# Optimization experiments

Hardware: AMD Instinct MI355X
Metric: run time of the kernel (lower is better)

Reference implementation:

```python
import jax, jax.numpy as jnp
import numpy as np

EMB = 512
N_ROWS = 10000
N_PAIRS = 65536


def setup_inputs() -> dict:
    key = jax.random.key(0)
    ks = jax.random.split(key, 10)
    s1 = 1.0 / np.sqrt(2 * EMB)
    s2 = 1.0 / np.sqrt(128)
    s3 = 1.0 / np.sqrt(64)
    return {
        "pos_pairs": jax.random.randint(ks[0], (N_PAIRS, 3), 0, N_ROWS, dtype=jnp.int32),
        "neg_pairs": jax.random.randint(ks[1], (N_PAIRS, 3), 0, N_ROWS, dtype=jnp.int32),
        "drug_embedding": jax.random.normal(ks[2], (N_ROWS, EMB), dtype=jnp.float32),
        "target_embedding": jax.random.normal(ks[3], (N_ROWS, EMB), dtype=jnp.float32),
        "W1": jax.random.normal(ks[4], (2 * EMB, 128), dtype=jnp.float32) * s1,
        "b1": jnp.zeros((128,), dtype=jnp.float32),
        "W2": jax.random.normal(ks[5], (128, 64), dtype=jnp.float32) * s2,
        "b2": jnp.zeros((64,), dtype=jnp.float32),
        "W3": jax.random.normal(ks[6], (64, 1), dtype=jnp.float32) * s3,
        "b3": jnp.zeros((1,), dtype=jnp.float32),
    }


def _mlp(x, W1, b1, W2, b2, W3, b3):
    h = jax.nn.relu(x @ W1 + b1)
    h = jax.nn.relu(h @ W2 + b2)
    return (h @ W3 + b3)[..., 0]  # [N]


def _pair_loss(pairs, drug_emb, tgt_emb, W1, b1, W2, b2, W3, b3):
    d = drug_emb[pairs[:, 0]]            # [N, EMB]
    t1 = tgt_emb[pairs[:, 1]]            # [N, EMB]
    t2 = tgt_emb[pairs[:, 2]]            # [N, EMB]
    a1 = _mlp(jnp.concatenate([d, t1], axis=-1), W1, b1, W2, b2, W3, b3)
    a2 = _mlp(jnp.concatenate([d, t2], axis=-1), W1, b1, W2, b2, W3, b3)
    # per-pair MSE of scalar affinities = (a1 - a2)^2; mean over pairs
    return jnp.mean((a1 - a2) ** 2)


def reference(pos_pairs, neg_pairs, drug_embedding, target_embedding,
              W1, b1, W2, b2, W3, b3):
    pos = _pair_loss(pos_pairs, drug_embedding, target_embedding, W1, b1, W2, b2, W3, b3)
    neg = _pair_loss(neg_pairs, drug_embedding, target_embedding, W1, b1, W2, b2, W3, b3)
    return pos - neg
```

## Files before the change

### kernel.cpp

```cpp
#include <hip/hip_runtime.h>

#define EMB 512
#define NROWS 10000
#define NPAIRS 65536

typedef __bf16 bf16x8 __attribute__((ext_vector_type(8)));
typedef float  f32x4  __attribute__((ext_vector_type(4)));
typedef unsigned int u32x4 __attribute__((ext_vector_type(4)));

__device__ __forceinline__ void split2(float x0, float x1, unsigned* hw, unsigned* lw) {
    unsigned u0 = __float_as_uint(x0), u1 = __float_as_uint(x1);
    unsigned r0 = u0 + 0x7FFFu + ((u0 >> 16) & 1u);
    unsigned r1 = u1 + 0x7FFFu + ((u1 >> 16) & 1u);
    float h0 = __uint_as_float(r0 & 0xFFFF0000u);
    float h1 = __uint_as_float(r1 & 0xFFFF0000u);
    float l0 = x0 - h0, l1 = x1 - h1;
    unsigned v0 = __float_as_uint(l0), v1 = __float_as_uint(l1);
    unsigned s0 = v0 + 0x7FFFu + ((v0 >> 16) & 1u);
    unsigned s1 = v1 + 0x7FFFu + ((v1 >> 16) & 1u);
    *hw = (r0 >> 16) | (r1 & 0xFFFF0000u);
    *lw = (s0 >> 16) | (s1 & 0xFFFF0000u);
}

__global__ __launch_bounds__(256)
void k0_fragment(const float* __restrict__ W1, const float* __restrict__ W2,
                 unsigned short* __restrict__ W1Fhi, unsigned short* __restrict__ W1Flo,
                 unsigned short* __restrict__ W2Fhi, unsigned short* __restrict__ W2Flo)
{
    int e = blockIdx.x * 256 + threadIdx.x;
    float x;
    unsigned short *hp, *lp;
    if (e < 131072) {
        int i  = e & 7;
        int l  = (e >> 3) & 63;
        int nt = (e >> 9) & 7;
        int kt = (e >> 12) & 15;
        int t  = e >> 16;
        int k = kt * 32 + 8 * (l >> 4) + i;
        int n = nt * 16 + (l & 15);
        x = W1[(t * 512 + k) * 128 + n];
        hp = W1Fhi + e; lp = W1Flo + e;
    } else {
        int e2 = e - 131072;
        int i  = e2 & 7;
        int l  = (e2 >> 3) & 63;
        int nt = (e2 >> 9) & 3;
        int kt = e2 >> 11;
        int k = kt * 32 + 8 * (l >> 4) + i;
        int n = nt * 16 + (l & 15);
        x = W2[k * 64 + n];
        hp = W2Fhi + e2; lp = W2Flo + e2;
    }
    unsigned u = __float_as_uint(x);
    unsigned r = u + 0x7FFFu + ((u >> 16) & 1u);
    float hf = __uint_as_float(r & 0xFFFF0000u);
    float lf = x - hf;
    unsigned v = __float_as_uint(lf);
    unsigned s = v + 0x7FFFu + ((v >> 16) & 1u);
    *hp = (unsigned short)(r >> 16);
    *lp = (unsigned short)(s >> 16);
}

#define K1_TILES 625

__global__ __launch_bounds__(256, 4)
void k1_mfma(const float* __restrict__ drug, const float* __restrict__ tgt,
             const unsigned* __restrict__ W1Fhi, const unsigned* __restrict__ W1Flo,
             const float* __restrict__ b1,
             float* __restrict__ D, float* __restrict__ T)
{
    __shared__ unsigned short Ahi[16][512];
    __shared__ unsigned short Alo[16][512];

    int bid = blockIdx.x, tid = threadIdx.x;
    bool isT = bid >= K1_TILES;
    int rt = isT ? bid - K1_TILES : bid;
    const float* emb = isT ? tgt : drug;
    float* out = isT ? T : D;
    int row0 = rt * 16;

    int wave = tid >> 6, lane = tid & 63;
    int g = lane >> 4, lm = lane & 15;
    int ntb = wave * 2;

    float4 va[4][2];
    #pragma unroll
    for (int i = 0; i < 4; i++) {
        const float* src = emb + (size_t)(row0 + wave * 4 + i) * EMB + lane * 8;
        va[i][0] = *(const float4*)src;
        va[i][1] = *(const float4*)(src + 4);
    }
    #pragma unroll
    for (int i = 0; i < 4; i++) {
        int row = wave * 4 + i;
        unsigned h0, h1, h2, h3, l0, l1, l2, l3;
        split2(va[i][0].x, va[i][0].y, &h0, &l0);
        split2(va[i][0].z, va[i][0].w, &h1, &l1);
        split2(va[i][1].x, va[i][1].y, &h2, &l2);
        split2(va[i][1].z, va[i][1].w, &h3, &l3);
        u32x4 hq, lq;
        hq[0]=h0; hq[1]=h1; hq[2]=h2; hq[3]=h3;
        lq[0]=l0; lq[1]=l1; lq[2]=l2; lq[3]=l3;
        int c = lane ^ (row & 7);
        *(u32x4*)((char*)&Ahi[0][0] + row * 1024 + c * 16) = hq;
        *(u32x4*)((char*)&Alo[0][0] + row * 1024 + c * 16) = lq;
    }
    __syncthreads();

    const u32x4* BH = (const u32x4*)W1Fhi + (isT ? 8192 : 0);
    const u32x4* BL = (const u32x4*)W1Flo + (isT ? 8192 : 0);

    f32x4 acc[2];
    #pragma unroll
    for (int j = 0; j < 2; j++) { acc[j][0]=0.f; acc[j][1]=0.f; acc[j][2]=0.f; acc[j][3]=0.f; }

    #pragma unroll
    for (int kt = 0; kt < 16; kt++) {
        u32x4 bh0 = BH[(kt * 8 + ntb) * 64 + lane];
        u32x4 bh1 = BH[(kt * 8 + ntb + 1) * 64 + lane];
        u32x4 bl0 = BL[(kt * 8 + ntb) * 64 + lane];
        u32x4 bl1 = BL[(kt * 8 + ntb + 1) * 64 + lane];
        int c = (kt * 4 + g) ^ (lm & 7);
        u32x4 ahq = *(const u32x4*)((const char*)&Ahi[0][0] + lm * 1024 + c * 16);
        u32x4 alq = *(const u32x4*)((const char*)&Alo[0][0] + lm * 1024 + c * 16);
        bf16x8 Ah = __builtin_bit_cast(bf16x8, ahq);
        bf16x8 Al = __builtin_bit_cast(bf16x8, alq);
        bf16x8 Bh0 = __builtin_bit_cast(bf16x8, bh0);
        bf16x8 Bh1 = __builtin_bit_cast(bf16x8, bh1);
        bf16x8 Bl0 = __builtin_bit_cast(bf16x8, bl0);
        bf16x8 Bl1 = __builtin_bit_cast(bf16x8, bl1);
        acc[0] = __builtin_amdgcn_mfma_f32_16x16x32_bf16(Ah, Bh0, acc[0], 0, 0, 0);
        acc[1] = __builtin_amdgcn_mfma_f32_16x16x32_bf16(Ah, Bh1, acc[1], 0, 0, 0);
        acc[0] = __builtin_amdgcn_mfma_f32_16x16x32_bf16(Ah, Bl0, acc[0], 0, 0, 0);
        acc[1] = __builtin_amdgcn_mfma_f32_16x16x32_bf16(Ah, Bl1, acc[1], 0, 0, 0);
        acc[0] = __builtin_amdgcn_mfma_f32_16x16x32_bf16(Al, Bh0, acc[0], 0, 0, 0);
        acc[1] = __builtin_amdgcn_mfma_f32_16x16x32_bf16(Al, Bh1, acc[1], 0, 0, 0);
    }

    #pragma unroll
    for (int j = 0; j < 2; j++) {
        int col = (ntb + j) * 16 + lm;
        float bias = isT ? 0.f : b1[col];
        #pragma unroll
        for (int reg = 0; reg < 4; reg++) {
            int row = row0 + 4 * g + reg;
            out[row * 128 + col] = acc[j][reg] + bias;
        }
    }
}

__global__ __launch_bounds__(256)
void k2_pairs(const float* __restrict__ D, const float* __restrict__ T,
              const int* __restrict__ pos, const int* __restrict__ neg,
              const unsigned* __restrict__ W2Fhi, const unsigned* __restrict__ W2Flo,
              const float* __restrict__ b2, const float* __restrict__ W3,
              double* __restrict__ partials)
{
    __shared__ u32x4 Ash[4][768];

    int tid = threadIdx.x;
    int wave = tid >> 6, lane = tid & 63;
    int g = lane >> 4, lm = lane & 15;
    int rr = lane >> 3, cc = lane & 7;
    int gw = blockIdx.x * 4 + wave;
    const int* pairs = (gw < 2048) ? pos : neg;
    int p0 = (gw & 2047) * 32;

    const float* bp[12];
    #pragma unroll
    for (int it = 0; it < 12; it++) {
        int pr = it * 8 + rr;
        int idxv;
        const float* src;
        if (pr < 32) { idxv = pairs[(p0 + pr) * 3]; src = D; }
        else { int q = pr - 32; idxv = pairs[(p0 + (q >> 1)) * 3 + 1 + (q & 1)]; src = T; }
        bp[it] = src + (size_t)idxv * 128 + ((cc ^ (pr & 7)) << 2);
    }

    u32x4* A4w = &Ash[wave][0];
    const u32x4* BH4 = (const u32x4*)W2Fhi;
    const u32x4* BL4 = (const u32x4*)W2Flo;

    f32x4 acc[4][4];
    #pragma unroll
    for (int mt = 0; mt < 4; mt++)
        #pragma unroll
        for (int nt = 0; nt < 4; nt++) { acc[mt][nt][0]=0.f; acc[mt][nt][1]=0.f; acc[mt][nt][2]=0.f; acc[mt][nt][3]=0.f; }

    #pragma unroll 1
    for (int kt = 0; kt < 4; kt++) {
        u32x4 bh[4], bl[4];
        #pragma unroll
        for (int nt = 0; nt < 4; nt++) {
            bh[nt] = BH4[(kt * 4 + nt) * 64 + lane];
            bl[nt] = BL4[(kt * 4 + nt) * 64 + lane];
        }
        #pragma unroll
        for (int it = 0; it < 12; it++) {
            __builtin_amdgcn_global_load_lds(
                (const __attribute__((address_space(1))) void*)(bp[it] + kt * 32),
                (__attribute__((address_space(3))) void*)((char*)A4w + it * 1024),
                16, 0, 0);
        }
        asm volatile("s_waitcnt vmcnt(0)" ::: "memory");
        #pragma unroll
        for (int mt = 0; mt < 4; mt++) {
            int r = mt * 16 + lm;
            int p = r >> 1;
            int ds = p & 7, ts = r & 7;
            const f32x4* drow = (const f32x4*)(A4w + p * 8);
            const f32x4* trow = (const f32x4*)(A4w + (32 + r) * 8);
            f32x4 d0 = drow[(2 * g) ^ ds];
            f32x4 d1 = drow[(2 * g + 1) ^ ds];
            f32x4 t0 = trow[(2 * g) ^ ts];
            f32x4 t1 = trow[(2 * g + 1) ^ ts];
            float h0 = fmaxf(d0[0] + t0[0], 0.f), h1v = fmaxf(d0[1] + t0[1], 0.f);
            float h2 = fmaxf(d0[2] + t0[2], 0.f), h3 = fmaxf(d0[3] + t0[3], 0.f);
            float h4 = fmaxf(d1[0] + t1[0], 0.f), h5 = fmaxf(d1[1] + t1[1], 0.f);
            float h6 = fmaxf(d1[2] + t1[2], 0.f), h7 = fmaxf(d1[3] + t1[3], 0.f);
            unsigned hq0, hq1, hq2, hq3, lq0, lq1, lq2, lq3;
            split2(h0, h1v, &hq0, &lq0);
            split2(h2, h3,  &hq1, &lq1);
            split2(h4, h5,  &hq2, &lq2);
            split2(h6, h7,  &hq3, &lq3);
            u32x4 ah, al;
            ah[0]=hq0; ah[1]=hq1; ah[2]=hq2; ah[3]=hq3;
            al[0]=lq0; al[1]=lq1; al[2]=lq2; al[3]=lq3;
            bf16x8 Ah = __builtin_bit_cast(bf16x8, ah);
            bf16x8 Al = __builtin_bit_cast(bf16x8, al);
            #pragma unroll
            for (int nt = 0; nt < 4; nt++) {
                bf16x8 Bh = __builtin_bit_cast(bf16x8, bh[nt]);
                bf16x8 Bl = __builtin_bit_cast(bf16x8, bl[nt]);
                acc[mt][nt] = __builtin_amdgcn_mfma_f32_16x16x32_bf16(Ah, Bh, acc[mt][nt], 0, 0, 0);
                acc[mt][nt] = __builtin_amdgcn_mfma_f32_16x16x32_bf16(Ah, Bl, acc[mt][nt], 0, 0, 0);
                acc[mt][nt] = __builtin_amdgcn_mfma_f32_16x16x32_bf16(Al, Bh, acc[mt][nt], 0, 0, 0);
            }
        }
        asm volatile("s_waitcnt lgkmcnt(0)" ::: "memory");
    }

    float b2v[4], w3v[4];
    #pragma unroll
    for (int nt = 0; nt < 4; nt++) { b2v[nt] = b2[nt * 16 + lm]; w3v[nt] = W3[nt * 16 + lm]; }

    float pr[4][4];
    #pragma unroll
    for (int mt = 0; mt < 4; mt++)
        #pragma unroll
        for (int reg = 0; reg < 4; reg++) {
            float s = 0.f;
            #pragma unroll
            for (int nt = 0; nt < 4; nt++) {
                float h2 = fmaxf(acc[mt][nt][reg] + b2v[nt], 0.f);
                s = fmaf(h2, w3v[nt], s);
            }
            pr[mt][reg] = s;
        }
    #pragma unroll
    for (int m = 1; m <= 8; m <<= 1)
        #pragma unroll
        for (int mt = 0; mt < 4; mt++)
            #pragma unroll
            for (int reg = 0; reg < 4; reg++)
                pr[mt][reg] += __shfl_xor(pr[mt][reg], m, 64);

    double dsq = 0.0;
    #pragma unroll
    for (int mt = 0; mt < 4; mt++) {
        float d0 = pr[mt][0] - pr[mt][1];
        float d1 = pr[mt][2] - pr[mt][3];
        dsq += (double)d0 * (double)d0 + (double)d1 * (double)d1;
    }
    dsq += __shfl_xor(dsq, 16, 64);
    dsq += __shfl_xor(dsq, 32, 64);

    __syncthreads();
    if (lane == 0) ((double*)&Ash[wave][0])[0] = dsq;
    __syncthreads();
    if (tid == 0) {
        double sum = 0.0;
        #pragma unroll
        for (int w = 0; w < 4; w++) sum += ((double*)&Ash[w][0])[0];
        partials[blockIdx.x] = sum;
    }
}

__global__ void k3_final(const double* __restrict__ partials, float* __restrict__ out)
{
    int lane = threadIdx.x;
    double sp = 0.0, sn = 0.0;
    #pragma unroll
    for (int i = 0; i < 8; i++) {
        sp += partials[lane + 64 * i];
        sn += partials[512 + lane + 64 * i];
    }
    #pragma unroll
    for (int m = 1; m <= 32; m <<= 1) {
        sp += __shfl_xor(sp, m, 64);
        sn += __shfl_xor(sn, m, 64);
    }
    if (lane == 0) out[0] = (float)((sp - sn) / (double)NPAIRS);
}

extern "C" void kernel_launch(void* const* d_in, const int* in_sizes, int n_in,
                              void* d_out, int out_size, void* d_ws, size_t ws_size,
                              hipStream_t stream) {
    const int*   pos  = (const int*)d_in[0];
    const int*   neg  = (const int*)d_in[1];
    const float* drug = (const float*)d_in[2];
    const float* tgt  = (const float*)d_in[3];
    const float* W1   = (const float*)d_in[4];
    const float* b1   = (const float*)d_in[5];
    const float* W2   = (const float*)d_in[6];
    const float* b2   = (const float*)d_in[7];
    const float* W3   = (const float*)d_in[8];

    float* Dp = (float*)d_ws;
    float* Tp = Dp + NROWS * 128;
    char* base = (char*)(Tp + NROWS * 128);
    unsigned short* W2Fhi = (unsigned short*)base;
    unsigned short* W2Flo = W2Fhi + 8192;
    unsigned short* W1Fhi = W2Flo + 8192;
    unsigned short* W1Flo = W1Fhi + 131072;
    double* partials = (double*)(W1Flo + 131072);
    float* out = (float*)d_out;

    k0_fragment<<<544, 256, 0, stream>>>(W1, W2, W1Fhi, W1Flo, W2Fhi, W2Flo);
    k1_mfma<<<2 * K1_TILES, 256, 0, stream>>>(drug, tgt, (const unsigned*)W1Fhi,
                                              (const unsigned*)W1Flo, b1, Dp, Tp);
    k2_pairs<<<1024, 256, 0, stream>>>(Dp, Tp, pos, neg, (const unsigned*)W2Fhi,
                                       (const unsigned*)W2Flo, b2, W3, partials);
    k3_final<<<1, 64, 0, stream>>>(partials, out);
}
```

Measured before the change: 60.10 us.

## Keep W1 fragments in registers across multiple row chunks with double-buffered LDS

Result: faster. 58.03 us (-3.4%).

```diff
diff --git a/kernel.cpp b/kernel.cpp
--- a/kernel.cpp
+++ b/kernel.cpp
@@ -61,91 +61,104 @@
     *lp = (unsigned short)(s >> 16);
 }
 
-#define K1_TILES 625
-
-__global__ __launch_bounds__(256, 4)
+#define K1_RPB 79
+#define K1_NCH 5
+
+__global__ __launch_bounds__(256, 2)
 void k1_mfma(const float* __restrict__ drug, const float* __restrict__ tgt,
              const unsigned* __restrict__ W1Fhi, const unsigned* __restrict__ W1Flo,
              const float* __restrict__ b1,
              float* __restrict__ D, float* __restrict__ T)
 {
-    __shared__ unsigned short Ahi[16][512];
-    __shared__ unsigned short Alo[16][512];
+    __shared__ unsigned short Ah[2][16][512];
+    __shared__ unsigned short Al[2][16][512];
 
     int bid = blockIdx.x, tid = threadIdx.x;
-    bool isT = bid >= K1_TILES;
-    int rt = isT ? bid - K1_TILES : bid;
-    const float* emb = isT ? tgt : drug;
-    float* out = isT ? T : D;
-    int row0 = rt * 16;
+    int t  = bid & 1;
+    int ch = (bid >> 1) & 1;
+    int rg = bid >> 2;
+    const float* emb = t ? tgt : drug;
+    float* out = t ? T : D;
+    int row_base = rg * K1_RPB;
 
     int wave = tid >> 6, lane = tid & 63;
     int g = lane >> 4, lm = lane & 15;
-    int ntb = wave * 2;
+    int nt = ch * 4 + wave;
+
+    const u32x4* BH = (const u32x4*)W1Fhi + (t ? 8192 : 0);
+    const u32x4* BL = (const u32x4*)W1Flo + (t ? 8192 : 0);
+
+    u32x4 bhv[16], blv[16];
+    #pragma unroll
+    for (int kt = 0; kt < 16; kt++) {
+        bhv[kt] = BH[(kt * 8 + nt) * 64 + lane];
+        blv[kt] = BL[(kt * 8 + nt) * 64 + lane];
+    }
+    float bias = t ? 0.f : b1[nt * 16 + lm];
 
     float4 va[4][2];
     #pragma unroll
     for (int i = 0; i < 4; i++) {
-        const float* src = emb + (size_t)(row0 + wave * 4 + i) * EMB + lane * 8;
+        int gr = row_base + 0 * 16 + wave * 4 + i;
+        if (gr > NROWS - 1) gr = NROWS - 1;
+        const float* src = emb + (size_t)gr * EMB + lane * 8;
         va[i][0] = *(const float4*)src;
         va[i][1] = *(const float4*)(src + 4);
     }
-    #pragma unroll
-    for (int i = 0; i < 4; i++) {
-        int row = wave * 4 + i;
-        unsigned h0, h1, h2, h3, l0, l1, l2, l3;
-        split2(va[i][0].x, va[i][0].y, &h0, &l0);
-        split2(va[i][0].z, va[i][0].w, &h1, &l1);
-        split2(va[i][1].x, va[i][1].y, &h2, &l2);
-        split2(va[i][1].z, va[i][1].w, &h3, &l3);
-        u32x4 hq, lq;
-        hq[0]=h0; hq[1]=h1; hq[2]=h2; hq[3]=h3;
-        lq[0]=l0; lq[1]=l1; lq[2]=l2; lq[3]=l3;
-        int c = lane ^ (row & 7);
-        *(u32x4*)((char*)&Ahi[0][0] + row * 1024 + c * 16) = hq;
-        *(u32x4*)((char*)&Alo[0][0] + row * 1024 + c * 16) = lq;
-    }
-    __syncthreads();
-
-    const u32x4* BH = (const u32x4*)W1Fhi + (isT ? 8192 : 0);
-    const u32x4* BL = (const u32x4*)W1Flo + (isT ? 8192 : 0);
-
-    f32x4 acc[2];
-    #pragma unroll
-    for (int j = 0; j < 2; j++) { acc[j][0]=0.f; acc[j][1]=0.f; acc[j][2]=0.f; acc[j][3]=0.f; }
-
-    #pragma unroll
-    for (int kt = 0; kt < 16; kt++) {
-        u32x4 bh0 = BH[(kt * 8 + ntb) * 64 + lane];
-        u32x4 bh1 = BH[(kt * 8 + ntb + 1) * 64 + lane];
-        u32x4 bl0 = BL[(kt * 8 + ntb) * 64 + lane];
-        u32x4 bl1 = BL[(kt * 8 + ntb + 1) * 64 + lane];
-        int c = (kt * 4 + g) ^ (lm & 7);
-        u32x4 ahq = *(const u32x4*)((const char*)&Ahi[0][0] + lm * 1024 + c * 16);
-        u32x4 alq = *(const u32x4*)((const char*)&Alo[0][0] + lm * 1024 + c * 16);
-        bf16x8 Ah = __builtin_bit_cast(bf16x8, ahq);
-        bf16x8 Al = __builtin_bit_cast(bf16x8, alq);
-        bf16x8 Bh0 = __builtin_bit_cast(bf16x8, bh0);
-        bf16x8 Bh1 = __builtin_bit_cast(bf16x8, bh1);
-        bf16x8 Bl0 = __builtin_bit_cast(bf16x8, bl0);
-        bf16x8 Bl1 = __builtin_bit_cast(bf16x8, bl1);
-        acc[0] = __builtin_amdgcn_mfma_f32_16x16x32_bf16(Ah, Bh0, acc[0], 0, 0, 0);
-        acc[1] = __builtin_amdgcn_mfma_f32_16x16x32_bf16(Ah, Bh1, acc[1], 0, 0, 0);
-        acc[0] = __builtin_amdgcn_mfma_f32_16x16x32_bf16(Ah, Bl0, acc[0], 0, 0, 0);
-        acc[1] = __builtin_amdgcn_mfma_f32_16x16x32_bf16(Ah, Bl1, acc[1], 0, 0, 0);
-        acc[0] = __builtin_amdgcn_mfma_f32_16x16x32_bf16(Al, Bh0, acc[0], 0, 0, 0);
-        acc[1] = __builtin_amdgcn_mfma_f32_16x16x32_bf16(Al, Bh1, acc[1], 0, 0, 0);
-    }
-
-    #pragma unroll
-    for (int j = 0; j < 2; j++) {
-        int col = (ntb + j) * 16 + lm;
-        float bias = isT ? 0.f : b1[col];
+
+    #pragma unroll
+    for (int c = 0; c < K1_NCH; c++) {
+        float4 vb[4][2];
+        if (c + 1 < K1_NCH) {
+            #pragma unroll
+            for (int i = 0; i < 4; i++) {
+                int gr = row_base + (c + 1) * 16 + wave * 4 + i;
+                if (gr > NROWS - 1) gr = NROWS - 1;
+                const float* src = emb + (size_t)gr * EMB + lane * 8;
+                vb[i][0] = *(const float4*)src;
+                vb[i][1] = *(const float4*)(src + 4);
+            }
+        }
+        #pragma unroll
+        for (int i = 0; i < 4; i++) {
+            int lr = wave * 4 + i;
+            unsigned h0, h1, h2, h3, l0, l1, l2, l3;
+            split2(va[i][0].x, va[i][0].y, &h0, &l0);
+            split2(va[i][0].z, va[i][0].w, &h1, &l1);
+            split2(va[i][1].x, va[i][1].y, &h2, &l2);
+            split2(va[i][1].z, va[i][1].w, &h3, &l3);
+            u32x4 hq, lq;
+            hq[0]=h0; hq[1]=h1; hq[2]=h2; hq[3]=h3;
+            lq[0]=l0; lq[1]=l1; lq[2]=l2; lq[3]=l3;
+            int cc = lane ^ (lr & 7);
+            *(u32x4*)((char*)&Ah[c & 1][0][0] + lr * 1024 + cc * 16) = hq;
+            *(u32x4*)((char*)&Al[c & 1][0][0] + lr * 1024 + cc * 16) = lq;
+        }
+        __syncthreads();
+        f32x4 acc;
+        acc[0]=0.f; acc[1]=0.f; acc[2]=0.f; acc[3]=0.f;
+        #pragma unroll
+        for (int kt = 0; kt < 16; kt++) {
+            int cc = (kt * 4 + g) ^ (lm & 7);
+            u32x4 ahq = *(const u32x4*)((const char*)&Ah[c & 1][0][0] + lm * 1024 + cc * 16);
+            u32x4 alq = *(const u32x4*)((const char*)&Al[c & 1][0][0] + lm * 1024 + cc * 16);
+            bf16x8 Af = __builtin_bit_cast(bf16x8, ahq);
+            bf16x8 Alf = __builtin_bit_cast(bf16x8, alq);
+            bf16x8 Bh = __builtin_bit_cast(bf16x8, bhv[kt]);
+            bf16x8 Bl = __builtin_bit_cast(bf16x8, blv[kt]);
+            acc = __builtin_amdgcn_mfma_f32_16x16x32_bf16(Af, Bh, acc, 0, 0, 0);
+            acc = __builtin_amdgcn_mfma_f32_16x16x32_bf16(Af, Bl, acc, 0, 0, 0);
+            acc = __builtin_amdgcn_mfma_f32_16x16x32_bf16(Alf, Bh, acc, 0, 0, 0);
+        }
         #pragma unroll
         for (int reg = 0; reg < 4; reg++) {
-            int row = row0 + 4 * g + reg;
-            out[row * 128 + col] = acc[j][reg] + bias;
-        }
+            int lr = c * 16 + 4 * g + reg;
+            int row = row_base + lr;
+            if (lr < K1_RPB && row < NROWS)
+                out[row * 128 + nt * 16 + lm] = acc[reg] + bias;
+        }
+        #pragma unroll
+        for (int i = 0; i < 4; i++) { va[i][0] = vb[i][0]; va[i][1] = vb[i][1]; }
     }
 }
 
@@ -226,15 +239,15 @@
             u32x4 ah, al;
             ah[0]=hq0; ah[1]=hq1; ah[2]=hq2; ah[3]=hq3;
             al[0]=lq0; al[1]=lq1; al[2]=lq2; al[3]=lq3;
-            bf16x8 Ah = __builtin_bit_cast(bf16x8, ah);
-            bf16x8 Al = __builtin_bit_cast(bf16x8, al);
+            bf16x8 Ahf = __builtin_bit_cast(bf16x8, ah);
+            bf16x8 Alf = __builtin_bit_cast(bf16x8, al);
             #pragma unroll
             for (int nt = 0; nt < 4; nt++) {
                 bf16x8 Bh = __builtin_bit_cast(bf16x8, bh[nt]);
                 bf16x8 Bl = __builtin_bit_cast(bf16x8, bl[nt]);
-                acc[mt][nt] = __builtin_amdgcn_mfma_f32_16x16x32_bf16(Ah, Bh, acc[mt][nt], 0, 0, 0);
-                acc[mt][nt] = __builtin_amdgcn_mfma_f32_16x16x32_bf16(Ah, Bl, acc[mt][nt], 0, 0, 0);
-                acc[mt][nt] = __builtin_amdgcn_mfma_f32_16x16x32_bf16(Al, Bh, acc[mt][nt], 0, 0, 0);
+                acc[mt][nt] = __builtin_amdgcn_mfma_f32_16x16x32_bf16(Ahf, Bh, acc[mt][nt], 0, 0, 0);
+                acc[mt][nt] = __builtin_amdgcn_mfma_f32_16x16x32_bf16(Ahf, Bl, acc[mt][nt], 0, 0, 0);
+                acc[mt][nt] = __builtin_amdgcn_mfma_f32_16x16x32_bf16(Alf, Bh, acc[mt][nt], 0, 0, 0);
             }
         }
         asm volatile("s_waitcnt lgkmcnt(0)" ::: "memory");
@@ -327,8 +340,8 @@
     float* out = (float*)d_out;
 
     k0_fragment<<<544, 256, 0, stream>>>(W1, W2, W1Fhi, W1Flo, W2Fhi, W2Flo);
-    k1_mfma<<<2 * K1_TILES, 256, 0, stream>>>(drug, tgt, (const unsigned*)W1Fhi,
-                                              (const unsigned*)W1Flo, b1, Dp, Tp);
+    k1_mfma<<<512, 256, 0, stream>>>(drug, tgt, (const unsigned*)W1Fhi,
+                                     (const unsigned*)W1Flo, b1, Dp, Tp);
     k2_pairs<<<1024, 256, 0, stream>>>(Dp, Tp, pos, neg, (const unsigned*)W2Fhi,
                                        (const unsigned*)W2Flo, b2, W3, partials);
     k3_final<<<1, 64, 0, stream>>>(partials, out);
```

## Stream k1 A tiles via global_load_lds per K step with in-loop bf16 split

Applied to the files above, without the earlier changes.

After: 60.60 us. About the same (+0.8%).

```diff
diff --git a/kernel.cpp b/kernel.cpp
--- a/kernel.cpp
+++ b/kernel.cpp
@@ -63,14 +63,13 @@
 
 #define K1_TILES 625
 
-__global__ __launch_bounds__(256, 4)
-void k1_mfma(const float* __restrict__ drug, const float* __restrict__ tgt,
-             const unsigned* __restrict__ W1Fhi, const unsigned* __restrict__ W1Flo,
-             const float* __restrict__ b1,
-             float* __restrict__ D, float* __restrict__ T)
+__global__ __launch_bounds__(256)
+void k1_dma(const float* __restrict__ drug, const float* __restrict__ tgt,
+            const unsigned* __restrict__ W1Fhi, const unsigned* __restrict__ W1Flo,
+            const float* __restrict__ b1,
+            float* __restrict__ D, float* __restrict__ T)
 {
-    __shared__ unsigned short Ahi[16][512];
-    __shared__ unsigned short Alo[16][512];
+    __shared__ u32x4 Abuf[4][128];
 
     int bid = blockIdx.x, tid = threadIdx.x;
     bool isT = bid >= K1_TILES;
@@ -81,50 +80,53 @@
 
     int wave = tid >> 6, lane = tid & 63;
     int g = lane >> 4, lm = lane & 15;
+    int rr = lane >> 3, cc = lane & 7;
     int ntb = wave * 2;
-
-    float4 va[4][2];
-    #pragma unroll
-    for (int i = 0; i < 4; i++) {
-        const float* src = emb + (size_t)(row0 + wave * 4 + i) * EMB + lane * 8;
-        va[i][0] = *(const float4*)src;
-        va[i][1] = *(const float4*)(src + 4);
-    }
-    #pragma unroll
-    for (int i = 0; i < 4; i++) {
-        int row = wave * 4 + i;
-        unsigned h0, h1, h2, h3, l0, l1, l2, l3;
-        split2(va[i][0].x, va[i][0].y, &h0, &l0);
-        split2(va[i][0].z, va[i][0].w, &h1, &l1);
-        split2(va[i][1].x, va[i][1].y, &h2, &l2);
-        split2(va[i][1].z, va[i][1].w, &h3, &l3);
-        u32x4 hq, lq;
-        hq[0]=h0; hq[1]=h1; hq[2]=h2; hq[3]=h3;
-        lq[0]=l0; lq[1]=l1; lq[2]=l2; lq[3]=l3;
-        int c = lane ^ (row & 7);
-        *(u32x4*)((char*)&Ahi[0][0] + row * 1024 + c * 16) = hq;
-        *(u32x4*)((char*)&Alo[0][0] + row * 1024 + c * 16) = lq;
-    }
-    __syncthreads();
+    int rk = lm & 7;
 
     const u32x4* BH = (const u32x4*)W1Fhi + (isT ? 8192 : 0);
     const u32x4* BL = (const u32x4*)W1Flo + (isT ? 8192 : 0);
 
+    const float* sp[2];
+    #pragma unroll
+    for (int it = 0; it < 2; it++) {
+        int pr = it * 8 + rr;
+        sp[it] = emb + (size_t)(row0 + pr) * EMB + ((cc ^ (pr & 7)) << 2);
+    }
+
+    u32x4* A4w = &Abuf[wave][0];
+
     f32x4 acc[2];
     #pragma unroll
     for (int j = 0; j < 2; j++) { acc[j][0]=0.f; acc[j][1]=0.f; acc[j][2]=0.f; acc[j][3]=0.f; }
 
-    #pragma unroll
+    #pragma unroll 1
     for (int kt = 0; kt < 16; kt++) {
         u32x4 bh0 = BH[(kt * 8 + ntb) * 64 + lane];
         u32x4 bh1 = BH[(kt * 8 + ntb + 1) * 64 + lane];
         u32x4 bl0 = BL[(kt * 8 + ntb) * 64 + lane];
         u32x4 bl1 = BL[(kt * 8 + ntb + 1) * 64 + lane];
-        int c = (kt * 4 + g) ^ (lm & 7);
-        u32x4 ahq = *(const u32x4*)((const char*)&Ahi[0][0] + lm * 1024 + c * 16);
-        u32x4 alq = *(const u32x4*)((const char*)&Alo[0][0] + lm * 1024 + c * 16);
-        bf16x8 Ah = __builtin_bit_cast(bf16x8, ahq);
-        bf16x8 Al = __builtin_bit_cast(bf16x8, alq);
+        #pragma unroll
+        for (int it = 0; it < 2; it++) {
+            __builtin_amdgcn_global_load_lds(
+                (const __attribute__((address_space(1))) void*)(sp[it] + kt * 32),
+                (__attribute__((address_space(3))) void*)((char*)A4w + it * 1024),
+                16, 0, 0);
+        }
+        asm volatile("s_waitcnt vmcnt(0)" ::: "memory");
+        const f32x4* Af = (const f32x4*)A4w;
+        f32x4 a0 = Af[lm * 8 + ((2 * g)     ^ rk)];
+        f32x4 a1 = Af[lm * 8 + ((2 * g + 1) ^ rk)];
+        unsigned h0, h1, h2, h3, l0, l1, l2, l3;
+        split2(a0[0], a0[1], &h0, &l0);
+        split2(a0[2], a0[3], &h1, &l1);
+        split2(a1[0], a1[1], &h2, &l2);
+        split2(a1[2], a1[3], &h3, &l3);
+        u32x4 ah, al;
+        ah[0]=h0; ah[1]=h1; ah[2]=h2; ah[3]=h3;
+        al[0]=l0; al[1]=l1; al[2]=l2; al[3]=l3;
+        bf16x8 Ah = __builtin_bit_cast(bf16x8, ah);
+        bf16x8 Al = __builtin_bit_cast(bf16x8, al);
         bf16x8 Bh0 = __builtin_bit_cast(bf16x8, bh0);
         bf16x8 Bh1 = __builtin_bit_cast(bf16x8, bh1);
         bf16x8 Bl0 = __builtin_bit_cast(bf16x8, bl0);
@@ -135,6 +137,7 @@
         acc[1] = __builtin_amdgcn_mfma_f32_16x16x32_bf16(Ah, Bl1, acc[1], 0, 0, 0);
         acc[0] = __builtin_amdgcn_mfma_f32_16x16x32_bf16(Al, Bh0, acc[0], 0, 0, 0);
         acc[1] = __builtin_amdgcn_mfma_f32_16x16x32_bf16(Al, Bh1, acc[1], 0, 0, 0);
+        asm volatile("s_waitcnt lgkmcnt(0)" ::: "memory");
     }
 
     #pragma unroll
@@ -226,15 +229,15 @@
             u32x4 ah, al;
             ah[0]=hq0; ah[1]=hq1; ah[2]=hq2; ah[3]=hq3;
             al[0]=lq0; al[1]=lq1; al[2]=lq2; al[3]=lq3;
-            bf16x8 Ah = __builtin_bit_cast(bf16x8, ah);
-            bf16x8 Al = __builtin_bit_cast(bf16x8, al);
+            bf16x8 Ahf = __builtin_bit_cast(bf16x8, ah);
+            bf16x8 Alf = __builtin_bit_cast(bf16x8, al);
             #pragma unroll
             for (int nt = 0; nt < 4; nt++) {
                 bf16x8 Bh = __builtin_bit_cast(bf16x8, bh[nt]);
                 bf16x8 Bl = __builtin_bit_cast(bf16x8, bl[nt]);
-                acc[mt][nt] = __builtin_amdgcn_mfma_f32_16x16x32_bf16(Ah, Bh, acc[mt][nt], 0, 0, 0);
-                acc[mt][nt] = __builtin_amdgcn_mfma_f32_16x16x32_bf16(Ah, Bl, acc[mt][nt], 0, 0, 0);
-                acc[mt][nt] = __builtin_amdgcn_mfma_f32_16x16x32_bf16(Al, Bh, acc[mt][nt], 0, 0, 0);
+                acc[mt][nt] = __builtin_amdgcn_mfma_f32_16x16x32_bf16(Ahf, Bh, acc[mt][nt], 0, 0, 0);
+                acc[mt][nt] = __builtin_amdgcn_mfma_f32_16x16x32_bf16(Ahf, Bl, acc[mt][nt], 0, 0, 0);
+                acc[mt][nt] = __builtin_amdgcn_mfma_f32_16x16x32_bf16(Alf, Bh, acc[mt][nt], 0, 0, 0);
             }
         }
         asm volatile("s_waitcnt lgkmcnt(0)" ::: "memory");
@@ -327,8 +330,8 @@
     float* out = (float*)d_out;
 
     k0_fragment<<<544, 256, 0, stream>>>(W1, W2, W1Fhi, W1Flo, W2Fhi, W2Flo);
-    k1_mfma<<<2 * K1_TILES, 256, 0, stream>>>(drug, tgt, (const unsigned*)W1Fhi,
-                                              (const unsigned*)W1Flo, b1, Dp, Tp);
+    k1_dma<<<2 * K1_TILES, 256, 0, stream>>>(drug, tgt, (const unsigned*)W1Fhi,
+                                             (const unsigned*)W1Flo, b1, Dp, Tp);
     k2_pairs<<<1024, 256, 0, stream>>>(Dp, Tp, pos, neg, (const unsigned*)W2Fhi,
                                        (const unsigned*)W2Flo, b2, W3, partials);
     k3_final<<<1, 64, 0, stream>>>(partials, out);
```
